# Kernel tuning notes

Measured on AMD Instinct MI355X. Metric: run time of the kernel, lower is better.

The kernel has to match this reference:

```python
import jax, jax.numpy as jnp
import numpy as np
from jax import lax

D = 1024
N = 16


def setup_inputs() -> dict:
    key = jax.random.key(0)
    ks = jax.random.split(key, 8)
    sequence = jax.random.normal(ks[0], (2, 2048, D), dtype=jnp.float32)
    # A initialized as -arange(1, D+1) broadcast over N (as in the module)
    A = jnp.broadcast_to(-jnp.arange(1, D + 1, dtype=jnp.float32)[:, None], (D, N))
    lim_B = 1.0 / np.sqrt(D)
    W_B = jax.random.uniform(ks[1], (N, D), minval=-lim_B, maxval=lim_B, dtype=jnp.float32)
    b_B = jax.random.uniform(ks[2], (N,), minval=-lim_B, maxval=lim_B, dtype=jnp.float32)
    W_C = jax.random.uniform(ks[3], (N, D), minval=-lim_B, maxval=lim_B, dtype=jnp.float32)
    b_C = jax.random.uniform(ks[4], (N,), minval=-lim_B, maxval=lim_B, dtype=jnp.float32)
    W_Delta = jax.random.uniform(ks[5], (1, D), minval=-lim_B, maxval=lim_B, dtype=jnp.float32)
    b_Delta = jax.random.uniform(ks[6], (1,), minval=-lim_B, maxval=lim_B, dtype=jnp.float32)
    # bias_Delta = log(rand()/(0.1-0.001)+0.001) as in the module init
    u = jax.random.uniform(ks[7], (1,), dtype=jnp.float32)
    bias_Delta = jnp.log(u / (0.1 - 0.001) + 0.001)
    return {"sequence": sequence, "A": A, "W_B": W_B, "b_B": b_B,
            "W_C": W_C, "b_C": b_C, "W_Delta": W_Delta, "b_Delta": b_Delta,
            "bias_Delta": bias_Delta}


def reference(sequence, A, W_B, b_B, W_C, b_C, W_Delta, b_Delta, bias_Delta):
    # sequence: [B, L, D]; A: [D, N]
    Bm = sequence @ W_B.T + b_B                    # [B, L, N]
    Cm = sequence @ W_C.T + b_C                    # [B, L, N]
    Delta = jax.nn.softplus(sequence @ W_Delta.T + b_Delta + bias_Delta)  # [B, L, 1]
    # Discretization (ZOH): A_bar = exp(A * Delta), B_bar = A^-1 (A_bar - 1) B
    A_bar = jnp.exp(A[None, None] * Delta[..., None])          # [B, L, D, N]
    B_bar = (1.0 / A) * (A_bar - 1.0) * Bm[..., None, :]       # [B, L, D, N]

    def step(state, xs):
        Ab, Bb, x, c = xs  # [B,D,N], [B,D,N], [B,D], [B,N]
        state = state * Ab + x[..., None] * Bb
        y = jnp.einsum('bdn,bn->bd', state, c)
        return state, y

    xs = (jnp.moveaxis(A_bar, 1, 0), jnp.moveaxis(B_bar, 1, 0),
          jnp.moveaxis(sequence, 1, 0), jnp.moveaxis(Cm, 1, 0))
    init = jnp.zeros(sequence.shape[:-2] + (A.shape[0], A.shape[1]), dtype=sequence.dtype)
    _, ys = lax.scan(step, init, xs)               # ys: [L, B, D]
    return jnp.moveaxis(ys, 0, 1)                  # [B, L, D]
```

## Files before the change

### kernel.cpp

```cpp
#include <hip/hip_runtime.h>
#include <cstdint>

#define BB 2
#define LL 2048
#define DD 1024
#define NN 16

#define PB 4

__global__ __launch_bounds__(256) void k_proj(
    const float* __restrict__ seq,
    const float* __restrict__ W_B, const float* __restrict__ b_B,
    const float* __restrict__ W_C, const float* __restrict__ b_C,
    const float* __restrict__ W_D, const float* __restrict__ b_D,
    const float* __restrict__ bias_D,
    float* __restrict__ Bm, float* __restrict__ Cm, float* __restrict__ Dl)
{
    __shared__ float red[256 * 34];

    const int tid = threadIdx.x;
    const int r   = tid >> 6;
    const int ks  = tid & 63;
    const int row = blockIdx.x * PB + r;

    const float* srow = seq + (size_t)row * DD;
    float4 sv[4];
    #pragma unroll
    for (int q = 0; q < 4; ++q)
        sv[q] = *(const float4*)&srow[q * 256 + ks * 4];

    float pb[16], pc[16], pd;

    #pragma unroll
    for (int w = 0; w < 16; ++w) {
        const float* wr = W_B + (size_t)w * DD;
        float a = 0.f;
        #pragma unroll
        for (int q = 0; q < 4; ++q) {
            float4 wv = *(const float4*)&wr[q * 256 + ks * 4];
            a = fmaf(sv[q].x, wv.x, a); a = fmaf(sv[q].y, wv.y, a);
            a = fmaf(sv[q].z, wv.z, a); a = fmaf(sv[q].w, wv.w, a);
        }
        pb[w] = a;
    }
    #pragma unroll
    for (int w = 0; w < 16; ++w) {
        const float* wr = W_C + (size_t)w * DD;
        float a = 0.f;
        #pragma unroll
        for (int q = 0; q < 4; ++q) {
            float4 wv = *(const float4*)&wr[q * 256 + ks * 4];
            a = fmaf(sv[q].x, wv.x, a); a = fmaf(sv[q].y, wv.y, a);
            a = fmaf(sv[q].z, wv.z, a); a = fmaf(sv[q].w, wv.w, a);
        }
        pc[w] = a;
    }
    {
        float a = 0.f;
        #pragma unroll
        for (int q = 0; q < 4; ++q) {
            float4 wv = *(const float4*)&W_D[q * 256 + ks * 4];
            a = fmaf(sv[q].x, wv.x, a); a = fmaf(sv[q].y, wv.y, a);
            a = fmaf(sv[q].z, wv.z, a); a = fmaf(sv[q].w, wv.w, a);
        }
        pd = a;
    }

    float* myrow = &red[tid * 34];
    #pragma unroll
    for (int w = 0; w < 16; ++w) myrow[w]      = pb[w];
    #pragma unroll
    for (int w = 0; w < 16; ++w) myrow[16 + w] = pc[w];
    myrow[32] = pd;
    __syncthreads();

    if (tid < PB * 33) {
        int r_o = tid / 33;
        int w_o = tid - r_o * 33;
        const float* base = &red[(r_o * 64) * 34 + w_o];
        float s = 0.f;
        #pragma unroll
        for (int k = 0; k < 64; ++k) s += base[k * 34];
        int rg = blockIdx.x * PB + r_o;
        if (w_o < 16) {
            Bm[(size_t)rg * NN + w_o] = s + b_B[w_o];
        } else if (w_o < 32) {
            Cm[(size_t)rg * NN + (w_o - 16)] = s + b_C[w_o - 16];
        } else {
            float z = s + b_D[0] + bias_D[0];
            Dl[rg] = (z > 15.f) ? z : log1pf(__expf(z));
        }
    }
}

__global__ __launch_bounds__(256) void k_scan_local(
    const float* __restrict__ seq, const float* __restrict__ A,
    const float* __restrict__ Dl, const float* __restrict__ Bm,
    float* __restrict__ Gp, float* __restrict__ Sl, int C, int S)
{
    const int d = ((blockIdx.x & 3) << 8) | threadIdx.x;
    const int b = (blockIdx.x >> 2) & 1;
    const int c = blockIdx.x >> 3;

    const float A_d  = A[(size_t)d * NN];
    const float invA = 1.0f / A_d;

    float st[NN];
    #pragma unroll
    for (int n = 0; n < NN; ++n) st[n] = 0.f;
    float g = 1.f;

    const int l0 = c * S;
    const float*  xp = seq + ((size_t)b * LL + l0) * DD + d;
    const float*  dp = Dl + (size_t)b * LL + l0;
    const float4* bp = (const float4*)(Bm + ((size_t)b * LL + l0) * NN);

    for (int r0 = 0; r0 < S; r0 += 4) {
        float x4[4];
        #pragma unroll
        for (int i = 0; i < 4; ++i) x4[i] = xp[(size_t)(r0 + i) * DD];
        #pragma unroll
        for (int i = 0; i < 4; ++i) {
            const int rr = r0 + i;
            float delta = dp[rr];
            float4 b0 = bp[rr*4+0], b1 = bp[rr*4+1], b2 = bp[rr*4+2], b3 = bp[rr*4+3];
            float abar = __expf(A_d * delta);
            float u    = (abar - 1.f) * invA * x4[i];
            float bm[NN] = { b0.x,b0.y,b0.z,b0.w, b1.x,b1.y,b1.z,b1.w,
                             b2.x,b2.y,b2.z,b2.w, b3.x,b3.y,b3.z,b3.w };
            #pragma unroll
            for (int n = 0; n < NN; ++n) st[n] = fmaf(st[n], abar, u * bm[n]);
            g *= abar;
        }
    }

    Gp[((size_t)b * C + c) * DD + d] = g;
    float4* so = (float4*)(Sl + (((size_t)b * C + c) * DD + d) * NN);
    so[0] = make_float4(st[0],  st[1],  st[2],  st[3]);
    so[1] = make_float4(st[4],  st[5],  st[6],  st[7]);
    so[2] = make_float4(st[8],  st[9],  st[10], st[11]);
    so[3] = make_float4(st[12], st[13], st[14], st[15]);
}

__global__ __launch_bounds__(256) void k_prefix(
    float* __restrict__ Sl, const float* __restrict__ Gp, int C)
{
    int tid = blockIdx.x * 256 + threadIdx.x;
    int n  = tid & (NN - 1);
    int bd = tid >> 4;
    int b  = bd >> 10;
    int d  = bd & (DD - 1);

    const size_t cstride  = (size_t)DD * NN;
    float* s0 = Sl + ((size_t)b * C * DD + d) * NN + n;
    const float* g0 = Gp + (size_t)b * C * DD + d;

    float sprev = s0[0];
    int c = 1;
    const int peel = (C - 1) & 3;
    for (; c < 1 + peel; ++c) {
        sprev = fmaf(g0[(size_t)c * DD], sprev, s0[(size_t)c * cstride]);
        s0[(size_t)c * cstride] = sprev;
    }
    for (; c < C; c += 4) {
        float gv[4], s[4];
        #pragma unroll
        for (int i = 0; i < 4; ++i) {
            gv[i] = g0[(size_t)(c + i) * DD];
            s[i]  = s0[(size_t)(c + i) * cstride];
        }
        #pragma unroll
        for (int i = 0; i < 4; ++i) {
            sprev = fmaf(gv[i], sprev, s[i]);
            s0[(size_t)(c + i) * cstride] = sprev;
        }
    }
}

__global__ __launch_bounds__(256) void k_scan_out(
    const float* __restrict__ seq, const float* __restrict__ A,
    const float* __restrict__ Dl, const float* __restrict__ Bm,
    const float* __restrict__ Cm, const float* __restrict__ Sl,
    float* __restrict__ out, int C, int S)
{
    const int d = ((blockIdx.x & 3) << 8) | threadIdx.x;
    const int b = (blockIdx.x >> 2) & 1;
    const int c = blockIdx.x >> 3;

    const float A_d  = A[(size_t)d * NN];
    const float invA = 1.0f / A_d;

    float st[NN];
    if (c == 0) {
        #pragma unroll
        for (int n = 0; n < NN; ++n) st[n] = 0.f;
    } else {
        const float4* si = (const float4*)(
            Sl + (((size_t)b * C + (c - 1)) * DD + d) * NN);
        float4 v0 = si[0], v1 = si[1], v2 = si[2], v3 = si[3];
        st[0]=v0.x; st[1]=v0.y; st[2]=v0.z; st[3]=v0.w;
        st[4]=v1.x; st[5]=v1.y; st[6]=v1.z; st[7]=v1.w;
        st[8]=v2.x; st[9]=v2.y; st[10]=v2.z; st[11]=v2.w;
        st[12]=v3.x; st[13]=v3.y; st[14]=v3.z; st[15]=v3.w;
    }

    const int l0 = c * S;
    const float*  xp = seq + ((size_t)b * LL + l0) * DD + d;
    const float*  dp = Dl + (size_t)b * LL + l0;
    const float4* bp = (const float4*)(Bm + ((size_t)b * LL + l0) * NN);
    const float4* cp = (const float4*)(Cm + ((size_t)b * LL + l0) * NN);
    float* yp = out + ((size_t)b * LL + l0) * DD + d;

    for (int r0 = 0; r0 < S; r0 += 4) {
        float x4[4];
        #pragma unroll
        for (int i = 0; i < 4; ++i) x4[i] = xp[(size_t)(r0 + i) * DD];
        #pragma unroll
        for (int i = 0; i < 4; ++i) {
            const int rr = r0 + i;
            float delta = dp[rr];
            float4 b0 = bp[rr*4+0], b1 = bp[rr*4+1], b2 = bp[rr*4+2], b3 = bp[rr*4+3];
            float abar = __expf(A_d * delta);
            float u    = (abar - 1.f) * invA * x4[i];
            float bm[NN] = { b0.x,b0.y,b0.z,b0.w, b1.x,b1.y,b1.z,b1.w,
                             b2.x,b2.y,b2.z,b2.w, b3.x,b3.y,b3.z,b3.w };
            #pragma unroll
            for (int n = 0; n < NN; ++n) st[n] = fmaf(st[n], abar, u * bm[n]);

            float4 c0 = cp[rr*4+0], c1 = cp[rr*4+1], c2 = cp[rr*4+2], c3 = cp[rr*4+3];
            float cm[NN] = { c0.x,c0.y,c0.z,c0.w, c1.x,c1.y,c1.z,c1.w,
                             c2.x,c2.y,c2.z,c2.w, c3.x,c3.y,c3.z,c3.w };
            float y0 = 0.f, y1 = 0.f, y2 = 0.f, y3 = 0.f;
            #pragma unroll
            for (int n = 0; n < NN; n += 4) {
                y0 = fmaf(st[n+0], cm[n+0], y0);
                y1 = fmaf(st[n+1], cm[n+1], y1);
                y2 = fmaf(st[n+2], cm[n+2], y2);
                y3 = fmaf(st[n+3], cm[n+3], y3);
            }
            yp[(size_t)rr * DD] = (y0 + y1) + (y2 + y3);
        }
    }
}

extern "C" void kernel_launch(void* const* d_in, const int* in_sizes, int n_in,
                              void* d_out, int out_size, void* d_ws, size_t ws_size,
                              hipStream_t stream)
{
    const float* seq    = (const float*)d_in[0];
    const float* A      = (const float*)d_in[1];
    const float* W_B    = (const float*)d_in[2];
    const float* b_B    = (const float*)d_in[3];
    const float* W_C    = (const float*)d_in[4];
    const float* b_C    = (const float*)d_in[5];
    const float* W_D    = (const float*)d_in[6];
    const float* b_D    = (const float*)d_in[7];
    const float* bias_D = (const float*)d_in[8];
    float* out = (float*)d_out;
    float* ws  = (float*)d_ws;

    float* Bm = ws;
    float* Cm = Bm + (size_t)BB * LL * NN;
    float* Dl = Cm + (size_t)BB * LL * NN;
    float* Gp = Dl + (size_t)BB * LL;

    int C = 128;
    while (C > 1) {
        size_t need = ((size_t)BB * LL * NN * 2 + (size_t)BB * LL +
                       (size_t)BB * DD * C * (1 + NN)) * sizeof(float);
        if (need <= ws_size) break;
        C >>= 1;
    }
    int S = LL / C;
    float* Sl = Gp + (size_t)BB * DD * C;

    k_proj<<<(BB * LL) / PB, 256, 0, stream>>>(seq, W_B, b_B, W_C, b_C,
                                               W_D, b_D, bias_D, Bm, Cm, Dl);
    k_scan_local<<<(BB * DD * C) / 256, 256, 0, stream>>>(seq, A, Dl, Bm, Gp, Sl, C, S);
    k_prefix<<<(BB * DD * NN) / 256, 256, 0, stream>>>(Sl, Gp, C);
    k_scan_out<<<(BB * DD * C) / 256, 256, 0, stream>>>(seq, A, Dl, Bm, Cm, Sl, out, C, S);
}
```

Measured before the change: 65.38 us.

## Parallelize chunk prefix with in-block Hillis-Steele scan and stage B/C/Delta in LDS

The chunk-state prefix kernel changes from a sequential loop over 128 chunks per (b,d,n) thread to one block per (b,d) that loads all chunk states into shared memory and runs a log-step Hillis-Steele scan. The local and output scan kernels now stage the chunk's Bm, Cm and Delta rows in shared memory and preload all 16 sequence values up front, instead of issuing repeated global loads inside the loop. The chunk count is hardcoded to 128, which removes the workspace-size fallback. The parallel scan does more total work plus barriers, and the fixed chunk count assumes the workspace is large enough.

```diff
diff --git a/kernel.cpp b/kernel.cpp
--- a/kernel.cpp
+++ b/kernel.cpp
@@ -5,6 +5,8 @@
 #define LL 2048
 #define DD 1024
 #define NN 16
+#define CC 128
+#define SS 16
 
 #define PB 4
 
@@ -96,46 +98,51 @@
 __global__ __launch_bounds__(256) void k_scan_local(
     const float* __restrict__ seq, const float* __restrict__ A,
     const float* __restrict__ Dl, const float* __restrict__ Bm,
-    float* __restrict__ Gp, float* __restrict__ Sl, int C, int S)
-{
-    const int d = ((blockIdx.x & 3) << 8) | threadIdx.x;
+    float* __restrict__ Gp, float* __restrict__ Sl)
+{
+    __shared__ float  dlds[SS];
+    __shared__ float4 blds[SS * 4];
+
+    const int t = threadIdx.x;
+    const int d = ((blockIdx.x & 3) << 8) | t;
     const int b = (blockIdx.x >> 2) & 1;
     const int c = blockIdx.x >> 3;
+    const int l0 = c * SS;
+
+    const float4* bp = (const float4*)(Bm + ((size_t)b * LL + l0) * NN);
+    if (t < SS * 4)            blds[t]      = bp[t];
+    else if (t < SS * 4 + SS)  dlds[t - SS * 4] = Dl[(size_t)b * LL + l0 + (t - SS * 4)];
 
     const float A_d  = A[(size_t)d * NN];
     const float invA = 1.0f / A_d;
 
+    const float* xp = seq + ((size_t)b * LL + l0) * DD + d;
+    float x16[SS];
+    #pragma unroll
+    for (int i = 0; i < SS; ++i) x16[i] = xp[(size_t)i * DD];
+
     float st[NN];
     #pragma unroll
     for (int n = 0; n < NN; ++n) st[n] = 0.f;
     float g = 1.f;
 
-    const int l0 = c * S;
-    const float*  xp = seq + ((size_t)b * LL + l0) * DD + d;
-    const float*  dp = Dl + (size_t)b * LL + l0;
-    const float4* bp = (const float4*)(Bm + ((size_t)b * LL + l0) * NN);
-
-    for (int r0 = 0; r0 < S; r0 += 4) {
-        float x4[4];
-        #pragma unroll
-        for (int i = 0; i < 4; ++i) x4[i] = xp[(size_t)(r0 + i) * DD];
-        #pragma unroll
-        for (int i = 0; i < 4; ++i) {
-            const int rr = r0 + i;
-            float delta = dp[rr];
-            float4 b0 = bp[rr*4+0], b1 = bp[rr*4+1], b2 = bp[rr*4+2], b3 = bp[rr*4+3];
-            float abar = __expf(A_d * delta);
-            float u    = (abar - 1.f) * invA * x4[i];
-            float bm[NN] = { b0.x,b0.y,b0.z,b0.w, b1.x,b1.y,b1.z,b1.w,
-                             b2.x,b2.y,b2.z,b2.w, b3.x,b3.y,b3.z,b3.w };
-            #pragma unroll
-            for (int n = 0; n < NN; ++n) st[n] = fmaf(st[n], abar, u * bm[n]);
-            g *= abar;
-        }
-    }
-
-    Gp[((size_t)b * C + c) * DD + d] = g;
-    float4* so = (float4*)(Sl + (((size_t)b * C + c) * DD + d) * NN);
+    __syncthreads();
+
+    #pragma unroll
+    for (int r = 0; r < SS; ++r) {
+        float  delta = dlds[r];
+        float4 b0 = blds[r*4+0], b1 = blds[r*4+1], b2 = blds[r*4+2], b3 = blds[r*4+3];
+        float abar = __expf(A_d * delta);
+        float u    = (abar - 1.f) * invA * x16[r];
+        float bm[NN] = { b0.x,b0.y,b0.z,b0.w, b1.x,b1.y,b1.z,b1.w,
+                         b2.x,b2.y,b2.z,b2.w, b3.x,b3.y,b3.z,b3.w };
+        #pragma unroll
+        for (int n = 0; n < NN; ++n) st[n] = fmaf(st[n], abar, u * bm[n]);
+        g *= abar;
+    }
+
+    Gp[((size_t)b * CC + c) * DD + d] = g;
+    float4* so = (float4*)(Sl + (((size_t)b * CC + c) * DD + d) * NN);
     so[0] = make_float4(st[0],  st[1],  st[2],  st[3]);
     so[1] = make_float4(st[4],  st[5],  st[6],  st[7]);
     so[2] = make_float4(st[8],  st[9],  st[10], st[11]);
@@ -143,37 +150,48 @@
 }
 
 __global__ __launch_bounds__(256) void k_prefix(
-    float* __restrict__ Sl, const float* __restrict__ Gp, int C)
-{
-    int tid = blockIdx.x * 256 + threadIdx.x;
-    int n  = tid & (NN - 1);
-    int bd = tid >> 4;
-    int b  = bd >> 10;
-    int d  = bd & (DD - 1);
-
-    const size_t cstride  = (size_t)DD * NN;
-    float* s0 = Sl + ((size_t)b * C * DD + d) * NN + n;
-    const float* g0 = Gp + (size_t)b * C * DD + d;
-
-    float sprev = s0[0];
-    int c = 1;
-    const int peel = (C - 1) & 3;
-    for (; c < 1 + peel; ++c) {
-        sprev = fmaf(g0[(size_t)c * DD], sprev, s0[(size_t)c * cstride]);
-        s0[(size_t)c * cstride] = sprev;
-    }
-    for (; c < C; c += 4) {
-        float gv[4], s[4];
-        #pragma unroll
-        for (int i = 0; i < 4; ++i) {
-            gv[i] = g0[(size_t)(c + i) * DD];
-            s[i]  = s0[(size_t)(c + i) * cstride];
-        }
-        #pragma unroll
-        for (int i = 0; i < 4; ++i) {
-            sprev = fmaf(gv[i], sprev, s[i]);
-            s0[(size_t)(c + i) * cstride] = sprev;
-        }
+    float* __restrict__ Sl, const float* __restrict__ Gp)
+{
+    __shared__ float sA[CC * 16], sB[CC * 16];
+    __shared__ float gA[CC], gB[CC];
+
+    const int t = threadIdx.x;
+    const int d = blockIdx.x & (DD - 1);
+    const int b = blockIdx.x >> 10;
+    const int E = (CC * NN) >> 8;
+
+    for (int i = 0; i < E; ++i) {
+        const int e = i * 256 + t;
+        const int c = e >> 4, n = e & 15;
+        sA[e] = Sl[(((size_t)b * CC + c) * DD + d) * NN + n];
+    }
+    if (t < CC) gA[t] = Gp[((size_t)b * CC + t) * DD + d];
+    __syncthreads();
+
+    float* curS = sA; float* nxtS = sB;
+    float* curG = gA; float* nxtG = gB;
+    for (int dk = 1; dk < CC; dk <<= 1) {
+        for (int i = 0; i < E; ++i) {
+            const int e = i * 256 + t;
+            const int c = e >> 4;
+            float s = curS[e];
+            if (c >= dk) s = fmaf(curG[c], curS[e - (dk << 4)], s);
+            nxtS[e] = s;
+        }
+        if (t < CC) {
+            float g = curG[t];
+            if (t >= dk) g *= curG[t - dk];
+            nxtG[t] = g;
+        }
+        __syncthreads();
+        float* tp = curS; curS = nxtS; nxtS = tp;
+        tp = curG; curG = nxtG; nxtG = tp;
+    }
+
+    for (int i = 0; i < E; ++i) {
+        const int e = i * 256 + t;
+        const int c = e >> 4, n = e & 15;
+        Sl[(((size_t)b * CC + c) * DD + d) * NN + n] = curS[e];
     }
 }
 
@@ -181,14 +199,31 @@
     const float* __restrict__ seq, const float* __restrict__ A,
     const float* __restrict__ Dl, const float* __restrict__ Bm,
     const float* __restrict__ Cm, const float* __restrict__ Sl,
-    float* __restrict__ out, int C, int S)
-{
-    const int d = ((blockIdx.x & 3) << 8) | threadIdx.x;
+    float* __restrict__ out)
+{
+    __shared__ float  dlds[SS];
+    __shared__ float4 blds[SS * 4];
+    __shared__ float4 clds[SS * 4];
+
+    const int t = threadIdx.x;
+    const int d = ((blockIdx.x & 3) << 8) | t;
     const int b = (blockIdx.x >> 2) & 1;
     const int c = blockIdx.x >> 3;
+    const int l0 = c * SS;
+
+    const float4* bp = (const float4*)(Bm + ((size_t)b * LL + l0) * NN);
+    const float4* cp = (const float4*)(Cm + ((size_t)b * LL + l0) * NN);
+    if (t < SS * 4)                 blds[t] = bp[t];
+    else if (t < SS * 8)            clds[t - SS * 4] = cp[t - SS * 4];
+    else if (t < SS * 8 + SS)       dlds[t - SS * 8] = Dl[(size_t)b * LL + l0 + (t - SS * 8)];
 
     const float A_d  = A[(size_t)d * NN];
     const float invA = 1.0f / A_d;
+
+    const float* xp = seq + ((size_t)b * LL + l0) * DD + d;
+    float x16[SS];
+    #pragma unroll
+    for (int i = 0; i < SS; ++i) x16[i] = xp[(size_t)i * DD];
 
     float st[NN];
     if (c == 0) {
@@ -196,7 +231,7 @@
         for (int n = 0; n < NN; ++n) st[n] = 0.f;
     } else {
         const float4* si = (const float4*)(
-            Sl + (((size_t)b * C + (c - 1)) * DD + d) * NN);
+            Sl + (((size_t)b * CC + (c - 1)) * DD + d) * NN);
         float4 v0 = si[0], v1 = si[1], v2 = si[2], v3 = si[3];
         st[0]=v0.x; st[1]=v0.y; st[2]=v0.z; st[3]=v0.w;
         st[4]=v1.x; st[5]=v1.y; st[6]=v1.z; st[7]=v1.w;
@@ -204,42 +239,33 @@
         st[12]=v3.x; st[13]=v3.y; st[14]=v3.z; st[15]=v3.w;
     }
 
-    const int l0 = c * S;
-    const float*  xp = seq + ((size_t)b * LL + l0) * DD + d;
-    const float*  dp = Dl + (size_t)b * LL + l0;
-    const float4* bp = (const float4*)(Bm + ((size_t)b * LL + l0) * NN);
-    const float4* cp = (const float4*)(Cm + ((size_t)b * LL + l0) * NN);
     float* yp = out + ((size_t)b * LL + l0) * DD + d;
 
-    for (int r0 = 0; r0 < S; r0 += 4) {
-        float x4[4];
-        #pragma unroll
-        for (int i = 0; i < 4; ++i) x4[i] = xp[(size_t)(r0 + i) * DD];
-        #pragma unroll
-        for (int i = 0; i < 4; ++i) {
-            const int rr = r0 + i;
-            float delta = dp[rr];
-            float4 b0 = bp[rr*4+0], b1 = bp[rr*4+1], b2 = bp[rr*4+2], b3 = bp[rr*4+3];
-            float abar = __expf(A_d * delta);
-            float u    = (abar - 1.f) * invA * x4[i];
-            float bm[NN] = { b0.x,b0.y,b0.z,b0.w, b1.x,b1.y,b1.z,b1.w,
-                             b2.x,b2.y,b2.z,b2.w, b3.x,b3.y,b3.z,b3.w };
-            #pragma unroll
-            for (int n = 0; n < NN; ++n) st[n] = fmaf(st[n], abar, u * bm[n]);
-
-            float4 c0 = cp[rr*4+0], c1 = cp[rr*4+1], c2 = cp[rr*4+2], c3 = cp[rr*4+3];
-            float cm[NN] = { c0.x,c0.y,c0.z,c0.w, c1.x,c1.y,c1.z,c1.w,
-                             c2.x,c2.y,c2.z,c2.w, c3.x,c3.y,c3.z,c3.w };
-            float y0 = 0.f, y1 = 0.f, y2 = 0.f, y3 = 0.f;
-            #pragma unroll
-            for (int n = 0; n < NN; n += 4) {
-                y0 = fmaf(st[n+0], cm[n+0], y0);
-                y1 = fmaf(st[n+1], cm[n+1], y1);
-                y2 = fmaf(st[n+2], cm[n+2], y2);
-                y3 = fmaf(st[n+3], cm[n+3], y3);
-            }
-            yp[(size_t)rr * DD] = (y0 + y1) + (y2 + y3);
-        }
+    __syncthreads();
+
+    #pragma unroll
+    for (int r = 0; r < SS; ++r) {
+        float  delta = dlds[r];
+        float4 b0 = blds[r*4+0], b1 = blds[r*4+1], b2 = blds[r*4+2], b3 = blds[r*4+3];
+        float abar = __expf(A_d * delta);
+        float u    = (abar - 1.f) * invA * x16[r];
+        float bm[NN] = { b0.x,b0.y,b0.z,b0.w, b1.x,b1.y,b1.z,b1.w,
+                         b2.x,b2.y,b2.z,b2.w, b3.x,b3.y,b3.z,b3.w };
+        #pragma unroll
+        for (int n = 0; n < NN; ++n) st[n] = fmaf(st[n], abar, u * bm[n]);
+
+        float4 c0 = clds[r*4+0], c1 = clds[r*4+1], c2 = clds[r*4+2], c3 = clds[r*4+3];
+        float cm[NN] = { c0.x,c0.y,c0.z,c0.w, c1.x,c1.y,c1.z,c1.w,
+                         c2.x,c2.y,c2.z,c2.w, c3.x,c3.y,c3.z,c3.w };
+        float y0 = 0.f, y1 = 0.f, y2 = 0.f, y3 = 0.f;
+        #pragma unroll
+        for (int n = 0; n < NN; n += 4) {
+            y0 = fmaf(st[n+0], cm[n+0], y0);
+            y1 = fmaf(st[n+1], cm[n+1], y1);
+            y2 = fmaf(st[n+2], cm[n+2], y2);
+            y3 = fmaf(st[n+3], cm[n+3], y3);
+        }
+        yp[(size_t)r * DD] = (y0 + y1) + (y2 + y3);
     }
 }
 
@@ -263,20 +289,11 @@
     float* Cm = Bm + (size_t)BB * LL * NN;
     float* Dl = Cm + (size_t)BB * LL * NN;
     float* Gp = Dl + (size_t)BB * LL;
-
-    int C = 128;
-    while (C > 1) {
-        size_t need = ((size_t)BB * LL * NN * 2 + (size_t)BB * LL +
-                       (size_t)BB * DD * C * (1 + NN)) * sizeof(float);
-        if (need <= ws_size) break;
-        C >>= 1;
-    }
-    int S = LL / C;
-    float* Sl = Gp + (size_t)BB * DD * C;
+    float* Sl = Gp + (size_t)BB * CC * DD;
 
     k_proj<<<(BB * LL) / PB, 256, 0, stream>>>(seq, W_B, b_B, W_C, b_C,
                                                W_D, b_D, bias_D, Bm, Cm, Dl);
-    k_scan_local<<<(BB * DD * C) / 256, 256, 0, stream>>>(seq, A, Dl, Bm, Gp, Sl, C, S);
-    k_prefix<<<(BB * DD * NN) / 256, 256, 0, stream>>>(Sl, Gp, C);
-    k_scan_out<<<(BB * DD * C) / 256, 256, 0, stream>>>(seq, A, Dl, Bm, Cm, Sl, out, C, S);
-}
+    k_scan_local<<<(BB * DD * CC) / 256, 256, 0, stream>>>(seq, A, Dl, Bm, Gp, Sl);
+    k_prefix<<<BB * DD, 256, 0, stream>>>(Sl, Gp);
+    k_scan_out<<<(BB * DD * CC) / 256, 256, 0, stream>>>(seq, A, Dl, Bm, Cm, Sl, out);
+}
```

Measured after the change: 66.00 us. No clear change (+0.9%).
